# Optimization experiments

Measured on AMD Instinct MI355X. Metric: run time of the kernel, lower is better.

Reference implementation:

```python
import jax, jax.numpy as jnp
import numpy as np


def setup_inputs() -> dict:
    key = jax.random.key(0)
    ks = jax.random.split(key, 6)
    B, T, U, D, K, V = 4, 256, 64, 512, 512, 1000
    return {
        "enc_state": jax.random.normal(ks[0], (B, T, D), dtype=jnp.float32),
        "dec_state": jax.random.normal(ks[1], (B, U, D), dtype=jnp.float32),
        "W1": jax.random.normal(ks[2], (K, 2 * D), dtype=jnp.float32) * (1.0 / np.sqrt(2 * D)),
        "b1": jax.random.normal(ks[3], (K,), dtype=jnp.float32) * 0.01,
        "W2": jax.random.normal(ks[4], (V, K), dtype=jnp.float32) * (1.0 / np.sqrt(K)),
        "b2": jax.random.normal(ks[5], (V,), dtype=jnp.float32) * 0.01,
    }


def reference(enc_state, dec_state, W1, b1, W2, b2):
    # JointNet: Linear(concat(enc_bc, dec_bc)) -> tanh -> Linear.
    # Linear over the concat [enc; dec] equals split-weight matmuls broadcast-summed,
    # so we never materialize the [B,T,U,2D] concat tensor (same math).
    D_enc = enc_state.shape[-1]
    W1e, W1d = W1[:, :D_enc], W1[:, D_enc:]
    he = jnp.einsum('btd,kd->btk', enc_state, W1e)  # [B,T,K]
    hd = jnp.einsum('bud,kd->buk', dec_state, W1d)  # [B,U,K]
    h = jnp.tanh(he[:, :, None, :] + hd[:, None, :, :] + b1)  # [B,T,U,K]
    return jnp.einsum('btuk,vk->btuv', h, W2) + b2  # [B,T,U,V]
```

## Files before the change

kernel.cpp:

```cpp
#include <hip/hip_runtime.h>


typedef __bf16 bf16x8 __attribute__((ext_vector_type(8)));
typedef float  f32x4  __attribute__((ext_vector_type(4)));

#define B_   4
#define T_   256
#define U_   64
#define D_   512
#define K_   512
#define V_   1000
#define ROWS_ 65536L

__device__ __forceinline__ float tanh_fast(float x) {
    float e = __expf(2.0f * x);
    float r = __builtin_amdgcn_rcpf(e + 1.0f);
    return fmaf(-2.0f, r, 1.0f);
}

__device__ __forceinline__ void gl_lds16(const void* g, void* l) {
    __builtin_amdgcn_global_load_lds(
        (const __attribute__((address_space(1))) unsigned int*)g,
        (__attribute__((address_space(3))) unsigned int*)l,
        16, 0, 0);
}

__global__ __launch_bounds__(256) void w2conv_kernel(const float* __restrict__ W2,
                                                     __bf16* __restrict__ W2b) {
    int idx = (blockIdx.x * 256 + threadIdx.x) * 8;
    int v = idx >> 9;
    bf16x8 o;
    if (v < V_) {
        const f32x4* p = (const f32x4*)(W2 + idx);
        f32x4 a = p[0], b = p[1];
#pragma unroll
        for (int j = 0; j < 4; ++j) { o[j] = (__bf16)a[j]; o[4 + j] = (__bf16)b[j]; }
    } else {
#pragma unroll
        for (int j = 0; j < 8; ++j) o[j] = (__bf16)0.0f;
    }
    *(bf16x8*)(W2b + idx) = o;
}

__global__ __launch_bounds__(256) void stage1_kernel(const float* __restrict__ enc,
                                                     const float* __restrict__ dec,
                                                     const float* __restrict__ W1,
                                                     float* __restrict__ he,
                                                     float* __restrict__ hd) {
    const int ct = blockIdx.x;
    const int rt = blockIdx.y;
    const bool isDec = rt >= 16;
    const float* X = isDec ? (dec + (rt - 16) * 64 * D_) : (enc + rt * 64 * D_);
    const int   woff = isDec ? D_ : 0;
    float*      Y = isDec ? (hd + (rt - 16) * 64 * K_) : (he + rt * 64 * K_);
    const int   k0 = ct * 64;

    __shared__ __align__(16) __bf16 As[64][72];
    __shared__ __align__(16) __bf16 Bs[64][72];

    const int tid  = threadIdx.x;
    const int lane = tid & 63, w = tid >> 6;
    const int wm = (w >> 1) * 32, wn = (w & 1) * 32;
    const int q = lane >> 4, li = lane & 15;

    f32x4 acc[2][2] = {};

    for (int d0 = 0; d0 < D_; d0 += 64) {
        __syncthreads();
#pragma unroll
        for (int i = 0; i < 2; ++i) {
            int s = tid + i * 256;
            int r = s >> 3, kc = s & 7;
            const f32x4* xp = (const f32x4*)(X + r * D_ + d0 + kc * 8);
            f32x4 x0 = xp[0], x1 = xp[1];
            bf16x8 a;
#pragma unroll
            for (int j = 0; j < 4; ++j) { a[j] = (__bf16)x0[j]; a[4 + j] = (__bf16)x1[j]; }
            *(bf16x8*)&As[r][kc * 8] = a;
            const f32x4* wp = (const f32x4*)(W1 + (k0 + r) * (2 * D_) + woff + d0 + kc * 8);
            f32x4 w0 = wp[0], w1 = wp[1];
            bf16x8 b;
#pragma unroll
            for (int j = 0; j < 4; ++j) { b[j] = (__bf16)w0[j]; b[4 + j] = (__bf16)w1[j]; }
            *(bf16x8*)&Bs[r][kc * 8] = b;
        }
        __syncthreads();
#pragma unroll
        for (int kk = 0; kk < 64; kk += 32) {
            bf16x8 af[2], bfr[2];
#pragma unroll
            for (int mi = 0; mi < 2; ++mi) af[mi]  = *(const bf16x8*)&As[wm + mi * 16 + li][kk + q * 8];
#pragma unroll
            for (int ni = 0; ni < 2; ++ni) bfr[ni] = *(const bf16x8*)&Bs[wn + ni * 16 + li][kk + q * 8];
#pragma unroll
            for (int mi = 0; mi < 2; ++mi)
#pragma unroll
                for (int ni = 0; ni < 2; ++ni)
                    acc[mi][ni] = __builtin_amdgcn_mfma_f32_16x16x32_bf16(af[mi], bfr[ni], acc[mi][ni], 0, 0, 0);
        }
    }
#pragma unroll
    for (int mi = 0; mi < 2; ++mi)
#pragma unroll
        for (int ni = 0; ni < 2; ++ni) {
            int row0 = wm + mi * 16 + q * 4;
            int col  = k0 + wn + ni * 16 + li;
            float* yp = Y + row0 * K_ + col;
            yp[0 * K_] = acc[mi][ni][0];
            yp[1 * K_] = acc[mi][ni][1];
            yp[2 * K_] = acc[mi][ni][2];
            yp[3 * K_] = acc[mi][ni][3];
        }
}

__global__ __launch_bounds__(256) void h_kernel(const float* __restrict__ he,
                                                const float* __restrict__ hd,
                                                const float* __restrict__ b1,
                                                __bf16* __restrict__ h,
                                                long r0) {
    const int tid = threadIdx.x;
    const long rl = (long)blockIdx.x * 4 + (tid >> 6);
    const long r  = r0 + rl;
    const int  k8 = (tid & 63) * 8;
    const long het = r >> 6;
    const long hdr = (r >> 14) * 64 + (r & 63);
    const f32x4* hp = (const f32x4*)(he + het * K_ + k8);
    const f32x4* dp = (const f32x4*)(hd + hdr * K_ + k8);
    const f32x4* bp = (const f32x4*)(b1 + k8);
    f32x4 s0 = hp[0] + dp[0] + bp[0];
    f32x4 s1 = hp[1] + dp[1] + bp[1];
    bf16x8 o;
#pragma unroll
    for (int j = 0; j < 4; ++j) {
        o[j]     = (__bf16)tanh_fast(s0[j]);
        o[4 + j] = (__bf16)tanh_fast(s1[j]);
    }
    *(bf16x8*)(h + rl * K_ + k8) = o;
}

__global__ __launch_bounds__(256) void joint_kernel(const __bf16* __restrict__ h,
                                                    const __bf16* __restrict__ W2b,
                                                    const float* __restrict__ b2,
                                                    float* __restrict__ out,
                                                    long r0, int nrt, int swz) {
    int ct, rt;
    {
        const int d = blockIdx.x;
        if (swz) {
            const int xcd = d & 7;
            const int m   = d >> 3;
            ct = m & 7;
            rt = xcd * (nrt >> 3) + (m >> 3);
        } else {
            ct = d & 7;
            rt = d >> 3;
        }
    }

    __shared__ __align__(16) __bf16 As[128 * 64];
    __shared__ __align__(16) __bf16 Bs[128 * 64];

    const int tid  = threadIdx.x;
    const int lane = tid & 63, w = tid >> 6;
    const int wm = (w >> 1) * 64, wn = (w & 1) * 64;
    const int q = lane >> 4, li = lane & 15;

    const int srow = lane >> 3;
    const int scol = ((lane & 7) ^ (srow & 7)) * 8;
    const long aRow = (long)rt * 128 + w * 8 + srow;
    const long bRow = (long)ct * 128 + w * 8 + srow;
    const __bf16* aBase = h   + aRow * K_ + scol;
    const __bf16* bBase = W2b + bRow * K_ + scol;
    __bf16* aLds = As + w * 512;
    __bf16* bLds = Bs + w * 512;

    const int cswz0 = ((q ^ (li & 7)) * 16);
    const char* AsB = (const char*)As;
    const char* BsB = (const char*)Bs;

    f32x4 acc[4][4] = {};

    for (int k0 = 0; k0 < K_; k0 += 64) {
        __syncthreads();
#pragma unroll
        for (int i = 0; i < 4; ++i) {
            gl_lds16(aBase + (long)i * 32 * K_ + k0, aLds + i * 2048);
            gl_lds16(bBase + (long)i * 32 * K_ + k0, bLds + i * 2048);
        }
        __syncthreads();
#pragma unroll
        for (int kk = 0; kk < 2; ++kk) {
            const int cs = cswz0 ^ (kk << 6);
            bf16x8 af[4], bfr[4];
#pragma unroll
            for (int mi = 0; mi < 4; ++mi) af[mi]  = *(const bf16x8*)(AsB + (wm + mi * 16 + li) * 128 + cs);
#pragma unroll
            for (int ni = 0; ni < 4; ++ni) bfr[ni] = *(const bf16x8*)(BsB + (wn + ni * 16 + li) * 128 + cs);
#pragma unroll
            for (int mi = 0; mi < 4; ++mi)
#pragma unroll
                for (int ni = 0; ni < 4; ++ni)
                    acc[mi][ni] = __builtin_amdgcn_mfma_f32_16x16x32_bf16(af[mi], bfr[ni], acc[mi][ni], 0, 0, 0);
        }
    }

    const long rbase = r0 + (long)rt * 128 + wm;
#pragma unroll
    for (int ni = 0; ni < 4; ++ni) {
        int gv = ct * 128 + wn + ni * 16 + li;
        if (gv < V_) {
            float bb = b2[gv];
#pragma unroll
            for (int mi = 0; mi < 4; ++mi) {
                long rr = rbase + mi * 16 + q * 4;
                float* op = out + rr * V_ + gv;
                __builtin_nontemporal_store(acc[mi][ni][0] + bb, op + 0L * V_);
                __builtin_nontemporal_store(acc[mi][ni][1] + bb, op + 1L * V_);
                __builtin_nontemporal_store(acc[mi][ni][2] + bb, op + 2L * V_);
                __builtin_nontemporal_store(acc[mi][ni][3] + bb, op + 3L * V_);
            }
        }
    }
}

extern "C" void kernel_launch(void* const* d_in, const int* in_sizes, int n_in,
                              void* d_out, int out_size, void* d_ws, size_t ws_size,
                              hipStream_t stream) {
    const float* enc = (const float*)d_in[0];
    const float* dec = (const float*)d_in[1];
    const float* W1  = (const float*)d_in[2];
    const float* b1  = (const float*)d_in[3];
    const float* W2  = (const float*)d_in[4];
    const float* b2  = (const float*)d_in[5];
    float* out = (float*)d_out;

    float*  he  = (float*)d_ws;
    float*  hd  = he + 1024 * K_;
    __bf16* W2b = (__bf16*)(hd + 256 * K_);
    __bf16* h   = W2b + 1024 * K_;
    const size_t fixed = (size_t)(1024 + 256) * K_ * 4 + (size_t)1024 * K_ * 2;

    long chunk = 0;
    if (ws_size > fixed) chunk = (long)((ws_size - fixed) / (K_ * 2));
    if (chunk >= ROWS_) chunk = ROWS_;
    else if (chunk >= 1024) chunk &= ~1023L;
    else chunk &= ~127L;
    if (chunk < 128) chunk = 128;

    w2conv_kernel<<<dim3(256), dim3(256), 0, stream>>>(W2, W2b);
    stage1_kernel<<<dim3(8, 20), dim3(256), 0, stream>>>(enc, dec, W1, he, hd);
    for (long r0 = 0; r0 < ROWS_; r0 += chunk) {
        long rows = ROWS_ - r0 < chunk ? ROWS_ - r0 : chunk;
        int  nrt  = (int)(rows / 128);
        int  swz  = (nrt & 7) == 0 ? 1 : 0;
        h_kernel<<<dim3((int)(rows / 4)), dim3(256), 0, stream>>>(he, hd, b1, h, r0);
        joint_kernel<<<dim3(8 * nrt), dim3(256), 0, stream>>>(h, W2b, b2, out, r0, nrt, swz);
    }
}
```

Baseline: 429.4 us.

## Pipeline joint GEMM with 256x128 tiles, 8 waves and multi-buffered async LDS loads

```diff
diff --git a/kernel.cpp b/kernel.cpp
--- a/kernel.cpp
+++ b/kernel.cpp
@@ -138,11 +138,11 @@
     *(bf16x8*)(h + rl * K_ + k8) = o;
 }
 
-__global__ __launch_bounds__(256) void joint_kernel(const __bf16* __restrict__ h,
-                                                    const __bf16* __restrict__ W2b,
-                                                    const float* __restrict__ b2,
-                                                    float* __restrict__ out,
-                                                    long r0, int nrt, int swz) {
+__global__ __launch_bounds__(512, 2) void joint_kernel(const __bf16* __restrict__ h,
+                                                       const __bf16* __restrict__ W2b,
+                                                       const float* __restrict__ b2,
+                                                       float* __restrict__ out,
+                                                       long r0, int nrt, int swz) {
     int ct, rt;
     {
         const int d = blockIdx.x;
@@ -157,54 +157,104 @@
         }
     }
 
-    __shared__ __align__(16) __bf16 As[128 * 64];
-    __shared__ __align__(16) __bf16 Bs[128 * 64];
+    __shared__ __align__(16) __bf16 As[3 * 256 * 64];
+    __shared__ __align__(16) __bf16 Bs[2 * 128 * 64];
 
     const int tid  = threadIdx.x;
     const int lane = tid & 63, w = tid >> 6;
-    const int wm = (w >> 1) * 64, wn = (w & 1) * 64;
+    const int wm = (w & 3) * 64;
+    const int wn = (w >> 2) * 64;
     const int q = lane >> 4, li = lane & 15;
 
-    const int srow = lane >> 3;
-    const int scol = ((lane & 7) ^ (srow & 7)) * 8;
-    const long aRow = (long)rt * 128 + w * 8 + srow;
-    const long bRow = (long)ct * 128 + w * 8 + srow;
-    const __bf16* aBase = h   + aRow * K_ + scol;
-    const __bf16* bBase = W2b + bRow * K_ + scol;
-    __bf16* aLds = As + w * 512;
-    __bf16* bLds = Bs + w * 512;
-
-    const int cswz0 = ((q ^ (li & 7)) * 16);
-    const char* AsB = (const char*)As;
-    const char* BsB = (const char*)Bs;
+    const int tr  = tid >> 3;
+    const int swl = ((tid & 7) ^ (tr & 7)) * 8;
+    const __bf16* aG = h   + ((long)rt * 256 + tr) * K_ + swl;
+    const __bf16* bG = W2b + ((long)ct * 128 + tr) * K_ + swl;
+    char* AsC = (char*)As;
+    char* BsC = (char*)Bs;
+    const int ldsOff = tid * 16;
+
+    const int csk0 = (q ^ (li & 7)) * 16;
 
     f32x4 acc[4][4] = {};
 
-    for (int k0 = 0; k0 < K_; k0 += 64) {
-        __syncthreads();
-#pragma unroll
-        for (int i = 0; i < 4; ++i) {
-            gl_lds16(aBase + (long)i * 32 * K_ + k0, aLds + i * 2048);
-            gl_lds16(bBase + (long)i * 32 * K_ + k0, bLds + i * 2048);
-        }
-        __syncthreads();
-#pragma unroll
-        for (int kk = 0; kk < 2; ++kk) {
-            const int cs = cswz0 ^ (kk << 6);
-            bf16x8 af[4], bfr[4];
-#pragma unroll
-            for (int mi = 0; mi < 4; ++mi) af[mi]  = *(const bf16x8*)(AsB + (wm + mi * 16 + li) * 128 + cs);
-#pragma unroll
-            for (int ni = 0; ni < 4; ++ni) bfr[ni] = *(const bf16x8*)(BsB + (wn + ni * 16 + li) * 128 + cs);
-#pragma unroll
-            for (int mi = 0; mi < 4; ++mi)
+#pragma unroll
+    for (int j = 0; j < 2; ++j)
+        gl_lds16(bG + j * 64 * K_, BsC + j * 8192 + ldsOff);
+#pragma unroll
+    for (int j = 0; j < 4; ++j)
+        gl_lds16(aG + j * 64 * K_, AsC + j * 8192 + ldsOff);
+#pragma unroll
+    for (int j = 0; j < 4; ++j)
+        gl_lds16(aG + 64 + j * 64 * K_, AsC + 32768 + j * 8192 + ldsOff);
+
+#pragma unroll
+    for (int u = 0; u < 8; ++u) {
+        if (u < 7) asm volatile("s_waitcnt vmcnt(4) lgkmcnt(0)" ::: "memory");
+        else       asm volatile("s_waitcnt vmcnt(0) lgkmcnt(0)" ::: "memory");
+        __builtin_amdgcn_s_barrier();
+
+        const char* Ab = AsC + (u % 3) * 32768;
+        const char* Bb = BsC + (u & 1) * 16384;
+
+        if (u + 1 < 8) {
+#pragma unroll
+            for (int j = 0; j < 2; ++j)
+                gl_lds16(bG + (u + 1) * 64 + j * 64 * K_,
+                         BsC + ((u + 1) & 1) * 16384 + j * 8192 + ldsOff);
+        }
+        if (u + 2 < 8) {
+#pragma unroll
+            for (int j = 0; j < 2; ++j)
+                gl_lds16(aG + (u + 2) * 64 + j * 64 * K_,
+                         AsC + ((u + 2) % 3) * 32768 + j * 8192 + ldsOff);
+        }
+
+        bf16x8 bfr[4][2], af[2][2];
+#pragma unroll
+        for (int ni = 0; ni < 4; ++ni)
+#pragma unroll
+            for (int kk = 0; kk < 2; ++kk)
+                bfr[ni][kk] = *(const bf16x8*)(Bb + (wn + ni * 16 + li) * 128 + (csk0 ^ (kk << 6)));
+#pragma unroll
+        for (int mi = 0; mi < 2; ++mi)
+#pragma unroll
+            for (int kk = 0; kk < 2; ++kk)
+                af[mi][kk] = *(const bf16x8*)(Ab + (wm + mi * 16 + li) * 128 + (csk0 ^ (kk << 6)));
+        __builtin_amdgcn_s_setprio(1);
+#pragma unroll
+        for (int kk = 0; kk < 2; ++kk)
+#pragma unroll
+            for (int mi = 0; mi < 2; ++mi)
 #pragma unroll
                 for (int ni = 0; ni < 4; ++ni)
-                    acc[mi][ni] = __builtin_amdgcn_mfma_f32_16x16x32_bf16(af[mi], bfr[ni], acc[mi][ni], 0, 0, 0);
-        }
-    }
-
-    const long rbase = r0 + (long)rt * 128 + wm;
+                    acc[mi][ni] = __builtin_amdgcn_mfma_f32_16x16x32_bf16(af[mi][kk], bfr[ni][kk], acc[mi][ni], 0, 0, 0);
+        __builtin_amdgcn_s_setprio(0);
+
+        if (u + 2 < 8) {
+#pragma unroll
+            for (int j = 2; j < 4; ++j)
+                gl_lds16(aG + (u + 2) * 64 + j * 64 * K_,
+                         AsC + ((u + 2) % 3) * 32768 + j * 8192 + ldsOff);
+        }
+
+#pragma unroll
+        for (int mi = 0; mi < 2; ++mi)
+#pragma unroll
+            for (int kk = 0; kk < 2; ++kk)
+                af[mi][kk] = *(const bf16x8*)(Ab + (wm + (2 + mi) * 16 + li) * 128 + (csk0 ^ (kk << 6)));
+        __builtin_amdgcn_s_setprio(1);
+#pragma unroll
+        for (int kk = 0; kk < 2; ++kk)
+#pragma unroll
+            for (int mi = 0; mi < 2; ++mi)
+#pragma unroll
+                for (int ni = 0; ni < 4; ++ni)
+                    acc[2 + mi][ni] = __builtin_amdgcn_mfma_f32_16x16x32_bf16(af[mi][kk], bfr[ni][kk], acc[2 + mi][ni], 0, 0, 0);
+        __builtin_amdgcn_s_setprio(0);
+    }
+
+    const long rbase = r0 + (long)rt * 256 + wm;
 #pragma unroll
     for (int ni = 0; ni < 4; ++ni) {
         int gv = ct * 128 + wn + ni * 16 + li;
@@ -243,17 +293,17 @@
     long chunk = 0;
     if (ws_size > fixed) chunk = (long)((ws_size - fixed) / (K_ * 2));
     if (chunk >= ROWS_) chunk = ROWS_;
-    else if (chunk >= 1024) chunk &= ~1023L;
-    else chunk &= ~127L;
-    if (chunk < 128) chunk = 128;
+    else if (chunk >= 2048) chunk &= ~2047L;
+    else chunk &= ~255L;
+    if (chunk < 256) chunk = 256;
 
     w2conv_kernel<<<dim3(256), dim3(256), 0, stream>>>(W2, W2b);
     stage1_kernel<<<dim3(8, 20), dim3(256), 0, stream>>>(enc, dec, W1, he, hd);
     for (long r0 = 0; r0 < ROWS_; r0 += chunk) {
         long rows = ROWS_ - r0 < chunk ? ROWS_ - r0 : chunk;
-        int  nrt  = (int)(rows / 128);
+        int  nrt  = (int)(rows / 256);
         int  swz  = (nrt & 7) == 0 ? 1 : 0;
         h_kernel<<<dim3((int)(rows / 4)), dim3(256), 0, stream>>>(he, hd, b1, h, r0);
-        joint_kernel<<<dim3(8 * nrt), dim3(256), 0, stream>>>(h, W2b, b2, out, r0, nrt, swz);
-    }
-}
+        joint_kernel<<<dim3(8 * nrt), dim3(512), 0, stream>>>(h, W2b, b2, out, r0, nrt, swz);
+    }
+}
```

New measurement: 442.2 us. 1.03x slower.
